# Kernel optimization log

Hardware: AMD Instinct MI355X
Metric: run time of the kernel (lower is better)

Reference implementation:

```python
import jax, jax.numpy as jnp
import numpy as np

N, H, T, HID = 2, 8, 1024, 64
EMBED_DIM = H * HID  # 512, out_proj dim
EPS = 1e-6


def setup_inputs() -> dict:
    key = jax.random.key(0)
    kq, kk, kv, kw, kb = jax.random.split(key, 5)
    q = jax.random.normal(kq, (N, H, T, HID), jnp.float32)
    k = jax.random.normal(kk, (N, H, T, HID), jnp.float32)
    v = jax.random.normal(kv, (N, H, T, HID), jnp.float32)
    W_out = jax.random.normal(kw, (EMBED_DIM, EMBED_DIM), jnp.float32) / np.float32(np.sqrt(EMBED_DIM))
    b_out = jax.random.normal(kb, (EMBED_DIM,), jnp.float32) * 0.02
    return {"q": q, "k": k, "v": v, "W_out": W_out, "b_out": b_out}


def reference(q, k, v, W_out, b_out):
    # cosFormer attention, causal=True, act_fun='relu', has_outproj=True
    n, h, t, hid = q.shape
    nh = n * h
    m = t  # max(src_len, tgt_len)

    # q/k: permute(2,0,1,3).view(T,N,H*HID) -> relu -> view(-1,N*H,HID).transpose(0,1)
    # is equivalent to a direct reshape (N,H,T,HID)->(N*H,T,HID) since relu is elementwise.
    qr = jax.nn.relu(q).reshape(nh, t, hid)
    kr = jax.nn.relu(k).reshape(nh, t, hid)
    # v: original does v.view(-1, N*H, HID).transpose(0,1) WITHOUT permuting first
    # (reinterprets the (N,H,T,HID) buffer as (T, N*H, HID)); reproduce faithfully.
    vr = jnp.swapaxes(v.reshape(t, nh, hid), 0, 1)  # (NH, T, HID)

    # cos/sin position reweighting: weight_index = pi/2 * arange(1..m), used as /m
    idx = (np.float32(np.pi / 2) * jnp.arange(1, t + 1, dtype=q.dtype)) / m  # (T,)
    s = jnp.sin(idx)[None, :, None]
    c = jnp.cos(idx)[None, :, None]
    q_ = jnp.concatenate([qr * s, qr * c], axis=-1)  # (NH, T, 2*HID)
    k_ = jnp.concatenate([kr * s, kr * c], axis=-1)  # (NH, T, 2*HID)

    # causal path: cumulative outer products k_ (x) v, then contract with q_
    kv = jnp.einsum('nld,nlm->nldm', k_, vr)          # (NH, T, 2*HID, HID)
    kv_cum = jnp.cumsum(kv, axis=1)
    qkv = jnp.einsum('nld,nldm->nlm', q_, kv_cum)     # (NH, T, HID)
    k_cum = jnp.cumsum(k_, axis=1)
    denom = jnp.maximum(jnp.einsum('nld,nld->nl', q_, k_cum), EPS)
    attn = qkv / denom[..., None]                     # (NH, T, HID)

    # (NH,T,HID) -> (T,N,H*HID), out_proj, back to (N,H,T,HID)
    attn = jnp.swapaxes(attn, 0, 1).reshape(t, n, h * hid)
    attn = attn @ W_out.T + b_out
    context = attn.reshape(t, n, h, hid).transpose(1, 2, 0, 3)  # (N,H,T,HID)
    probs = jnp.zeros((n, h, t, t), q.dtype)
    return context, probs
```

## Files before the change

kernel.cpp:

```cpp
#include <hip/hip_runtime.h>

#define TSEQ 1024
#define HIDV 64
#define NHEADS 16
#define LCH 64
#define NCH 16
#define EMBED 512
#define CTX_FLOATS (NHEADS * TSEQ * HIDV)
#define PROBS_F4 ((size_t)4194304)
#define EPSV 1e-6f
#define PIH 1.5707963267948966f

typedef short bf16x8 __attribute__((ext_vector_type(8)));
typedef float f32x4 __attribute__((ext_vector_type(4)));

__device__ __forceinline__ float relu_f(float x) { return fmaxf(x, 0.0f); }
__device__ __forceinline__ ushort f2bf(float f) {
    uint u = __float_as_uint(f);
    u += 0x7FFF + ((u >> 16) & 1);
    return (ushort)(u >> 16);
}
__device__ __forceinline__ float bf2f(ushort h) { return __uint_as_float(((uint)h) << 16); }
__device__ __forceinline__ uint pk2(float a, float b) {
    return (uint)f2bf(a) | ((uint)f2bf(b) << 16);
}

__global__ __launch_bounds__(512) void k_chunksum(
    const float* __restrict__ K, const float* __restrict__ V,
    float* __restrict__ Sws, float* __restrict__ ksumws,
    float4* __restrict__ probs4)
{
    __shared__ ushort kwT[128 * 72];
    __shared__ ushort vT[64 * 72];
    const int blk = blockIdx.x;
    const int b = blk >> 4, c = blk & 15;
    const int l0 = c * LCH;
    const int tid = threadIdx.x;

    {
        float4 z = make_float4(0.f, 0.f, 0.f, 0.f);
        size_t zb = (size_t)blk * 4096 + tid;
        #pragma unroll
        for (int s = 0; s < 8; ++s) probs4[zb + s * 512] = z;
    }

    #pragma unroll
    for (int s = 0; s < 2; ++s) {
        int e = tid + s * 512;
        int i = e >> 4, d = (e & 15) * 4;
        float4 k4 = *(const float4*)(K + (size_t)(b * TSEQ + l0 + i) * HIDV + d);
        float ang = PIH * (float)(l0 + i + 1) * (1.0f / 1024.0f);
        float si = sinf(ang), ci = cosf(ang);
        float kv[4] = {relu_f(k4.x), relu_f(k4.y), relu_f(k4.z), relu_f(k4.w)};
        #pragma unroll
        for (int j = 0; j < 4; ++j) {
            kwT[(d + j) * 72 + i] = f2bf(si * kv[j]);
            kwT[(d + 64 + j) * 72 + i] = f2bf(ci * kv[j]);
        }
        float4 v4 = *(const float4*)(V + ((size_t)(l0 + i) * NHEADS + b) * HIDV + d);
        float vv[4] = {v4.x, v4.y, v4.z, v4.w};
        #pragma unroll
        for (int j = 0; j < 4; ++j) vT[(d + j) * 72 + i] = f2bf(vv[j]);
    }
    __syncthreads();

    const int w = tid >> 6, lane = tid & 63;
    const int quad = lane >> 4, l15 = lane & 15;
    const int it = w;

    bf16x8 af[2];
    #pragma unroll
    for (int kk = 0; kk < 2; ++kk)
        af[kk] = *(const bf16x8*)(kwT + (it * 16 + l15) * 72 + kk * 32 + quad * 8);

    f32x4 acc[4];
    #pragma unroll
    for (int mt = 0; mt < 4; ++mt) {
        acc[mt] = (f32x4){0.f, 0.f, 0.f, 0.f};
        #pragma unroll
        for (int kk = 0; kk < 2; ++kk) {
            bf16x8 bf = *(const bf16x8*)(vT + (mt * 16 + l15) * 72 + kk * 32 + quad * 8);
            acc[mt] = __builtin_amdgcn_mfma_f32_16x16x32_bf16(af[kk], bf, acc[mt], 0, 0, 0);
        }
    }
    float* Sp = Sws + (size_t)blk * 8192;
    #pragma unroll
    for (int mt = 0; mt < 4; ++mt)
        #pragma unroll
        for (int r = 0; r < 4; ++r)
            Sp[(it * 16 + quad * 4 + r) * 64 + mt * 16 + l15] = acc[mt][r];

    if (tid < 128) {
        float s = 0.f;
        #pragma unroll
        for (int ss = 0; ss < 8; ++ss) {
            uint4 u = *(const uint4*)(kwT + tid * 72 + ss * 8);
            s += bf2f((ushort)(u.x & 0xffff)) + bf2f((ushort)(u.x >> 16));
            s += bf2f((ushort)(u.y & 0xffff)) + bf2f((ushort)(u.y >> 16));
            s += bf2f((ushort)(u.z & 0xffff)) + bf2f((ushort)(u.z >> 16));
            s += bf2f((ushort)(u.w & 0xffff)) + bf2f((ushort)(u.w >> 16));
        }
        ksumws[(size_t)blk * 128 + tid] = s;
    }
}

__global__ __launch_bounds__(256) void k_scan(
    float* __restrict__ Sws, float* __restrict__ ksumws,
    float4* __restrict__ probs4)
{
    {
        float4 z = make_float4(0.f, 0.f, 0.f, 0.f);
        size_t zb = 1048576 + (size_t)blockIdx.x * 2048 + threadIdx.x;
        #pragma unroll
        for (int s = 0; s < 8; ++s) probs4[zb + s * 256] = z;
    }
    int g = blockIdx.x * 256 + threadIdx.x;
    int b = g >> 13, idx = g & 8191;
    float acc = 0.0f;
    #pragma unroll
    for (int c = 0; c < NCH; ++c) {
        float* p = Sws + ((size_t)(b * NCH + c)) * 8192 + idx;
        float t = *p; *p = acc; acc += t;
    }
    if (g < NHEADS * 128) {
        int b2 = g >> 7, i2 = g & 127;
        float a2 = 0.0f;
        #pragma unroll
        for (int c = 0; c < NCH; ++c) {
            float* p = ksumws + (size_t)(b2 * NCH + c) * 128 + i2;
            float t = *p; *p = a2; a2 += t;
        }
    }
}

__global__ __launch_bounds__(512) void k_attn(
    const float* __restrict__ Q, const float* __restrict__ K,
    const float* __restrict__ V,
    const float* __restrict__ Sws, const float* __restrict__ ksumws,
    float* __restrict__ attn2, float4* __restrict__ probs4)
{
    __shared__ ushort qw[64 * 136];
    __shared__ ushort kw[64 * 136];
    __shared__ ushort Pt[64 * 136];
    __shared__ ushort vT[64 * 72];
    __shared__ ushort Am[64 * 72];
    __shared__ float psum[128], denA[64], denI[64];

    const int blk = blockIdx.x;
    const int b = blk >> 4, c = blk & 15;
    const int l0 = c * LCH;
    const int tid = threadIdx.x;

    {
        float4 z = make_float4(0.f, 0.f, 0.f, 0.f);
        size_t zb = 2097152 + (size_t)blk * 4096 + tid;
        #pragma unroll
        for (int s = 0; s < 8; ++s) probs4[zb + s * 512] = z;
    }
    if (tid < 64) denA[tid] = 0.f;

    #pragma unroll
    for (int s = 0; s < 2; ++s) {
        int e = tid + s * 512;
        int i = e >> 4, d = (e & 15) * 4;
        float ang = PIH * (float)(l0 + i + 1) * (1.0f / 1024.0f);
        float si = sinf(ang), ci = cosf(ang);
        float4 q4 = *(const float4*)(Q + (size_t)(b * TSEQ + l0 + i) * HIDV + d);
        float qv[4] = {relu_f(q4.x), relu_f(q4.y), relu_f(q4.z), relu_f(q4.w)};
        *(uint2*)(qw + i * 136 + d) = make_uint2(pk2(si * qv[0], si * qv[1]), pk2(si * qv[2], si * qv[3]));
        *(uint2*)(qw + i * 136 + 64 + d) = make_uint2(pk2(ci * qv[0], ci * qv[1]), pk2(ci * qv[2], ci * qv[3]));
        float4 k4 = *(const float4*)(K + (size_t)(b * TSEQ + l0 + i) * HIDV + d);
        float kv[4] = {relu_f(k4.x), relu_f(k4.y), relu_f(k4.z), relu_f(k4.w)};
        *(uint2*)(kw + i * 136 + d) = make_uint2(pk2(si * kv[0], si * kv[1]), pk2(si * kv[2], si * kv[3]));
        *(uint2*)(kw + i * 136 + 64 + d) = make_uint2(pk2(ci * kv[0], ci * kv[1]), pk2(ci * kv[2], ci * kv[3]));
        float4 v4 = *(const float4*)(V + ((size_t)(l0 + i) * NHEADS + b) * HIDV + d);
        float vv[4] = {v4.x, v4.y, v4.z, v4.w};
        #pragma unroll
        for (int j = 0; j < 4; ++j) vT[(d + j) * 72 + i] = f2bf(vv[j]);
    }
    {
        const float* Pg = Sws + (size_t)blk * 8192;
        #pragma unroll
        for (int s = 0; s < 4; ++s) {
            int e = tid + s * 512;
            int dd = e >> 4, m = (e & 15) * 4;
            float4 p4 = *(const float4*)(Pg + dd * 64 + m);
            float pv[4] = {p4.x, p4.y, p4.z, p4.w};
            #pragma unroll
            for (int j = 0; j < 4; ++j) Pt[(m + j) * 136 + dd] = f2bf(pv[j]);
        }
        if (tid < 128) psum[tid] = ksumws[(size_t)blk * 128 + tid];
    }
    __syncthreads();

    const int w = tid >> 6, lane = tid & 63;
    const int quad = lane >> 4, l15 = lane & 15;
    const int it = w >> 1;
    const int jb = (w & 1) * 2;

    bf16x8 af[4];
    #pragma unroll
    for (int kk = 0; kk < 4; ++kk)
        af[kk] = *(const bf16x8*)(qw + (it * 16 + l15) * 136 + kk * 32 + quad * 8);

    f32x4 accA[2];
    #pragma unroll
    for (int jj = 0; jj < 2; ++jj) {
        accA[jj] = (f32x4){0.f, 0.f, 0.f, 0.f};
        #pragma unroll
        for (int kk = 0; kk < 4; ++kk) {
            bf16x8 bf = *(const bf16x8*)(kw + ((jb + jj) * 16 + l15) * 136 + kk * 32 + quad * 8);
            accA[jj] = __builtin_amdgcn_mfma_f32_16x16x32_bf16(af[kk], bf, accA[jj], 0, 0, 0);
        }
    }
    {
        float rsum[4] = {0.f, 0.f, 0.f, 0.f};
        #pragma unroll
        for (int jj = 0; jj < 2; ++jj) {
            int j = (jb + jj) * 16 + l15;
            #pragma unroll
            for (int r = 0; r < 4; ++r) {
                int i = it * 16 + quad * 4 + r;
                float val = (j <= i) ? accA[jj][r] : 0.f;
                Am[i * 72 + j] = f2bf(val);
                rsum[r] += val;
            }
        }
        #pragma unroll
        for (int off = 1; off < 16; off <<= 1) {
            rsum[0] += __shfl_xor(rsum[0], off);
            rsum[1] += __shfl_xor(rsum[1], off);
            rsum[2] += __shfl_xor(rsum[2], off);
            rsum[3] += __shfl_xor(rsum[3], off);
        }
        if (l15 == 0) {
            #pragma unroll
            for (int r = 0; r < 4; ++r)
                atomicAdd(&denA[it * 16 + quad * 4 + r], rsum[r]);
        }
    }
    if (tid < 64) {
        float s = 0.f;
        #pragma unroll
        for (int ss = 0; ss < 16; ++ss) {
            uint4 u = *(const uint4*)(qw + tid * 136 + ss * 8);
            s += bf2f((ushort)(u.x & 0xffff)) * psum[ss * 8 + 0] + bf2f((ushort)(u.x >> 16)) * psum[ss * 8 + 1];
            s += bf2f((ushort)(u.y & 0xffff)) * psum[ss * 8 + 2] + bf2f((ushort)(u.y >> 16)) * psum[ss * 8 + 3];
            s += bf2f((ushort)(u.z & 0xffff)) * psum[ss * 8 + 4] + bf2f((ushort)(u.z >> 16)) * psum[ss * 8 + 5];
            s += bf2f((ushort)(u.w & 0xffff)) * psum[ss * 8 + 6] + bf2f((ushort)(u.w >> 16)) * psum[ss * 8 + 7];
        }
        denI[tid] = s;
    }
    __syncthreads();

    f32x4 accO[2];
    #pragma unroll
    for (int mm = 0; mm < 2; ++mm) {
        accO[mm] = (f32x4){0.f, 0.f, 0.f, 0.f};
        #pragma unroll
        for (int kk = 0; kk < 4; ++kk) {
            bf16x8 bp = *(const bf16x8*)(Pt + ((jb + mm) * 16 + l15) * 136 + kk * 32 + quad * 8);
            accO[mm] = __builtin_amdgcn_mfma_f32_16x16x32_bf16(af[kk], bp, accO[mm], 0, 0, 0);
        }
    }
    bf16x8 aA[2];
    #pragma unroll
    for (int kk = 0; kk < 2; ++kk)
        aA[kk] = *(const bf16x8*)(Am + (it * 16 + l15) * 72 + kk * 32 + quad * 8);
    #pragma unroll
    for (int mm = 0; mm < 2; ++mm)
        #pragma unroll
        for (int kk = 0; kk < 2; ++kk) {
            bf16x8 bv = *(const bf16x8*)(vT + ((jb + mm) * 16 + l15) * 72 + kk * 32 + quad * 8);
            accO[mm] = __builtin_amdgcn_mfma_f32_16x16x32_bf16(aA[kk], bv, accO[mm], 0, 0, 0);
        }

    const int nb = b >> 3, hh = b & 7;
    #pragma unroll
    for (int r = 0; r < 4; ++r) {
        int i = it * 16 + quad * 4 + r;
        float inv = 1.0f / fmaxf(denA[i] + denI[i], EPSV);
        #pragma unroll
        for (int mm = 0; mm < 2; ++mm) {
            int m = (jb + mm) * 16 + l15;
            size_t row = (size_t)((l0 + i) * 2 + nb);
            attn2[row * EMBED + hh * 64 + m] = accO[mm][r] * inv;
        }
    }
}

__global__ __launch_bounds__(256) void k_outproj(
    const float* __restrict__ A2, const float* __restrict__ W,
    const float* __restrict__ bias, float* __restrict__ ctx,
    float4* __restrict__ probs4)
{
    __shared__ ushort Ab[64 * 72];
    __shared__ ushort Bb[64 * 72];
    const int r0 = blockIdx.x * 64;
    const int e0 = blockIdx.y * 64;
    const int tid = threadIdx.x;
    const int blin = blockIdx.y * 32 + blockIdx.x;

    {
        float4 z = make_float4(0.f, 0.f, 0.f, 0.f);
        size_t zb = 3145728 + (size_t)blin * 4096 + tid;
        #pragma unroll
        for (int s = 0; s < 16; ++s) probs4[zb + s * 256] = z;
    }

    const int w = tid >> 6, lane = tid & 63;
    const int quad = lane >> 4, l15 = lane & 15;
    const int it = w;
    f32x4 acc[4];
    #pragma unroll
    for (int jt = 0; jt < 4; ++jt) acc[jt] = (f32x4){0.f, 0.f, 0.f, 0.f};

    for (int f0 = 0; f0 < EMBED; f0 += 64) {
        __syncthreads();
        #pragma unroll
        for (int s = 0; s < 4; ++s) {
            int e = tid + s * 256;
            int rr = e >> 4, ff = (e & 15) * 4;
            float4 a4 = *(const float4*)(A2 + (size_t)(r0 + rr) * EMBED + f0 + ff);
            *(uint2*)(Ab + rr * 72 + ff) = make_uint2(pk2(a4.x, a4.y), pk2(a4.z, a4.w));
            float4 w4 = *(const float4*)(W + (size_t)(e0 + rr) * EMBED + f0 + ff);
            *(uint2*)(Bb + rr * 72 + ff) = make_uint2(pk2(w4.x, w4.y), pk2(w4.z, w4.w));
        }
        __syncthreads();
        bf16x8 af[2];
        #pragma unroll
        for (int kk = 0; kk < 2; ++kk)
            af[kk] = *(const bf16x8*)(Ab + (it * 16 + l15) * 72 + kk * 32 + quad * 8);
        #pragma unroll
        for (int jt = 0; jt < 4; ++jt)
            #pragma unroll
            for (int kk = 0; kk < 2; ++kk) {
                bf16x8 bf = *(const bf16x8*)(Bb + (jt * 16 + l15) * 72 + kk * 32 + quad * 8);
                acc[jt] = __builtin_amdgcn_mfma_f32_16x16x32_bf16(af[kk], bf, acc[jt], 0, 0, 0);
            }
    }
    #pragma unroll
    for (int jt = 0; jt < 4; ++jt) {
        int e = e0 + jt * 16 + l15;
        float be = bias[e];
        int h = e >> 6, m = e & 63;
        #pragma unroll
        for (int r = 0; r < 4; ++r) {
            int rr = r0 + it * 16 + quad * 4 + r;
            int t = rr >> 1, n = rr & 1;
            ctx[((size_t)(n * 8 + h) * TSEQ + t) * HIDV + m] = acc[jt][r] + be;
        }
    }
}

extern "C" void kernel_launch(void* const* d_in, const int* in_sizes, int n_in,
                              void* d_out, int out_size, void* d_ws, size_t ws_size,
                              hipStream_t stream) {
    const float* q = (const float*)d_in[0];
    const float* k = (const float*)d_in[1];
    const float* v = (const float*)d_in[2];
    const float* W = (const float*)d_in[3];
    const float* bias = (const float*)d_in[4];
    float* out = (float*)d_out;
    float* ws = (float*)d_ws;

    float* S_ws = ws;
    float* ksum_ws = ws + 2097152;
    float* attn2 = ws + 2097152 + 32768;
    float4* probs4 = (float4*)(out + CTX_FLOATS);

    k_chunksum<<<dim3(256), dim3(512), 0, stream>>>(k, v, S_ws, ksum_ws, probs4);
    k_scan<<<dim3(512), dim3(256), 0, stream>>>(S_ws, ksum_ws, probs4);
    k_attn<<<dim3(256), dim3(512), 0, stream>>>(q, k, v, S_ws, ksum_ws, attn2, probs4);
    k_outproj<<<dim3(32, 8), dim3(256), 0, stream>>>(attn2, W, bias, out, probs4);
}
```

Before: 121.4 us.

## Fuse four attention stages into one cooperative persistent kernel with grid syncs

Replaces the four separate launches (chunk sums, scan, attention, out-projection) with one cooperative kernel of 512 blocks that uses grid.sync between phases. The chunk state is stored in bf16 and pre-transposed, so the attention phase loads it with vector copies. Work per block is re-split: attention now splits the output columns across two blocks, and the probs zero-fill is spread over idle blocks. This removes launch gaps and halves intermediate traffic, at the cost of grid-wide barriers, an occupancy requirement for co-residency, and lower precision in the scanned prefix sums.

```diff
diff --git a/kernel.cpp b/kernel.cpp
--- a/kernel.cpp
+++ b/kernel.cpp
@@ -1,4 +1,7 @@
 #include <hip/hip_runtime.h>
+#include <hip/hip_cooperative_groups.h>
+
+namespace cg = cooperative_groups;
 
 #define TSEQ 1024
 #define HIDV 64
@@ -7,7 +10,6 @@
 #define NCH 16
 #define EMBED 512
 #define CTX_FLOATS (NHEADS * TSEQ * HIDV)
-#define PROBS_F4 ((size_t)4194304)
 #define EPSV 1e-6f
 #define PIH 1.5707963267948966f
 
@@ -25,331 +27,339 @@
     return (uint)f2bf(a) | ((uint)f2bf(b) << 16);
 }
 
-__global__ __launch_bounds__(512) void k_chunksum(
-    const float* __restrict__ K, const float* __restrict__ V,
-    float* __restrict__ Sws, float* __restrict__ ksumws,
+#define SMEM_BYTES 58368
+#define OFF_QW 0
+#define OFF_KW 17408
+#define OFF_PT 34816
+#define OFF_VT 43520
+#define OFF_AM 48128
+#define OFF_PSUM 57344
+#define OFF_DENA 57856
+#define OFF_DENI 58112
+
+__global__ __launch_bounds__(256) void k_fused(
+    const float* __restrict__ Q, const float* __restrict__ K,
+    const float* __restrict__ V, const float* __restrict__ W,
+    const float* __restrict__ bias, float* __restrict__ out,
+    ushort* __restrict__ S16, float* __restrict__ ksumws,
+    ushort* __restrict__ Ptg, float* __restrict__ attn2,
     float4* __restrict__ probs4)
 {
-    __shared__ ushort kwT[128 * 72];
-    __shared__ ushort vT[64 * 72];
-    const int blk = blockIdx.x;
-    const int b = blk >> 4, c = blk & 15;
-    const int l0 = c * LCH;
+    __shared__ __align__(16) char smem[SMEM_BYTES];
+    cg::grid_group grid = cg::this_grid();
+
+    const int bid = blockIdx.x;
     const int tid = threadIdx.x;
+    const int w = tid >> 6, lane = tid & 63;
+    const int quad = lane >> 4, l15 = lane & 15;
+
+    if (bid < 256) {
+        ushort* kwT = (ushort*)smem;
+        ushort* vT1 = (ushort*)(smem + 22528);
+        const int pair = bid;
+        const int b = pair >> 4, c = pair & 15;
+        const int l0 = c * LCH;
+
+        #pragma unroll
+        for (int s = 0; s < 4; ++s) {
+            int e = tid + s * 256;
+            int i = e >> 4, d = (e & 15) * 4;
+            float4 k4 = *(const float4*)(K + (size_t)(b * TSEQ + l0 + i) * HIDV + d);
+            float si, ci;
+            __sincosf(PIH * (float)(l0 + i + 1) * (1.0f / 1024.0f), &si, &ci);
+            float kv[4] = {relu_f(k4.x), relu_f(k4.y), relu_f(k4.z), relu_f(k4.w)};
+            #pragma unroll
+            for (int j = 0; j < 4; ++j) {
+                kwT[(d + j) * 88 + i] = f2bf(si * kv[j]);
+                kwT[(d + 64 + j) * 88 + i] = f2bf(ci * kv[j]);
+            }
+            float4 v4 = *(const float4*)(V + ((size_t)(l0 + i) * NHEADS + b) * HIDV + d);
+            float vv[4] = {v4.x, v4.y, v4.z, v4.w};
+            #pragma unroll
+            for (int j = 0; j < 4; ++j) vT1[(d + j) * 88 + i] = f2bf(vv[j]);
+        }
+        __syncthreads();
+
+        f32x4 acc[2][4];
+        #pragma unroll
+        for (int ii = 0; ii < 2; ++ii)
+            #pragma unroll
+            for (int mt = 0; mt < 4; ++mt) acc[ii][mt] = (f32x4){0.f, 0.f, 0.f, 0.f};
+        #pragma unroll
+        for (int ii = 0; ii < 2; ++ii) {
+            int itv = w + ii * 4;
+            bf16x8 af[2];
+            #pragma unroll
+            for (int kk = 0; kk < 2; ++kk)
+                af[kk] = *(const bf16x8*)(kwT + (itv * 16 + l15) * 88 + kk * 32 + quad * 8);
+            #pragma unroll
+            for (int mt = 0; mt < 4; ++mt)
+                #pragma unroll
+                for (int kk = 0; kk < 2; ++kk) {
+                    bf16x8 bf = *(const bf16x8*)(vT1 + (mt * 16 + l15) * 88 + kk * 32 + quad * 8);
+                    acc[ii][mt] = __builtin_amdgcn_mfma_f32_16x16x32_bf16(af[kk], bf, acc[ii][mt], 0, 0, 0);
+                }
+        }
+        ushort* SpT = S16 + (size_t)pair * 8192;
+        #pragma unroll
+        for (int ii = 0; ii < 2; ++ii)
+            #pragma unroll
+            for (int mt = 0; mt < 4; ++mt) {
+                int m = mt * 16 + l15;
+                int ddb = (w + ii * 4) * 16 + quad * 4;
+                uint2 pk = make_uint2(pk2(acc[ii][mt][0], acc[ii][mt][1]),
+                                      pk2(acc[ii][mt][2], acc[ii][mt][3]));
+                *(uint2*)(SpT + m * 128 + ddb) = pk;
+            }
+        if (tid < 128) {
+            float ssum = 0.f;
+            #pragma unroll
+            for (int ss = 0; ss < 8; ++ss) {
+                uint4 u = *(const uint4*)(kwT + tid * 88 + ss * 8);
+                ssum += bf2f((ushort)(u.x & 0xffff)) + bf2f((ushort)(u.x >> 16));
+                ssum += bf2f((ushort)(u.y & 0xffff)) + bf2f((ushort)(u.y >> 16));
+                ssum += bf2f((ushort)(u.z & 0xffff)) + bf2f((ushort)(u.z >> 16));
+                ssum += bf2f((ushort)(u.w & 0xffff)) + bf2f((ushort)(u.w >> 16));
+            }
+            ksumws[(size_t)pair * 128 + tid] = ssum;
+        }
+    } else {
+        float4 z = make_float4(0.f, 0.f, 0.f, 0.f);
+        size_t base = (size_t)(bid - 256) * 8192 + tid;
+        #pragma unroll
+        for (int s = 0; s < 32; ++s) probs4[base + s * 256] = z;
+    }
+
+    grid.sync();
+
+    {
+        int g = bid * 256 + tid;
+        int bs = g >> 13, idx = g & 8191;
+        const ushort* Sp = S16 + (size_t)bs * 131072 + idx;
+        ushort* Pp = Ptg + (size_t)bs * 131072 + idx;
+        float acc = 0.f;
+        #pragma unroll
+        for (int c = 0; c < NCH; ++c) {
+            float t = bf2f(Sp[c * 8192]);
+            Pp[c * 8192] = f2bf(acc);
+            acc += t;
+        }
+        if (g < NHEADS * 128) {
+            int b2 = g >> 7, i2 = g & 127;
+            float a2 = 0.f;
+            #pragma unroll
+            for (int c = 0; c < NCH; ++c) {
+                float* p = ksumws + (size_t)(b2 * NCH + c) * 128 + i2;
+                float t = *p; *p = a2; a2 += t;
+            }
+        }
+    }
+
+    grid.sync();
+
+    {
+        ushort* qw = (ushort*)(smem + OFF_QW);
+        ushort* kw = (ushort*)(smem + OFF_KW);
+        ushort* Pt = (ushort*)(smem + OFF_PT);
+        ushort* vT = (ushort*)(smem + OFF_VT);
+        ushort* Am = (ushort*)(smem + OFF_AM);
+        float* psum = (float*)(smem + OFF_PSUM);
+        float* denA = (float*)(smem + OFF_DENA);
+        float* denI = (float*)(smem + OFF_DENI);
+
+        const int pair = bid >> 1, mh = bid & 1, m0b = mh * 32;
+        const int b = pair >> 4, c = pair & 15;
+        const int l0 = c * LCH;
+
+        #pragma unroll
+        for (int s = 0; s < 4; ++s) {
+            int e = tid + s * 256;
+            int i = e >> 4, d = (e & 15) * 4;
+            float si, ci;
+            __sincosf(PIH * (float)(l0 + i + 1) * (1.0f / 1024.0f), &si, &ci);
+            float4 q4 = *(const float4*)(Q + (size_t)(b * TSEQ + l0 + i) * HIDV + d);
+            float qv[4] = {relu_f(q4.x), relu_f(q4.y), relu_f(q4.z), relu_f(q4.w)};
+            *(uint2*)(qw + i * 136 + d) = make_uint2(pk2(si * qv[0], si * qv[1]), pk2(si * qv[2], si * qv[3]));
+            *(uint2*)(qw + i * 136 + 64 + d) = make_uint2(pk2(ci * qv[0], ci * qv[1]), pk2(ci * qv[2], ci * qv[3]));
+            float4 k4 = *(const float4*)(K + (size_t)(b * TSEQ + l0 + i) * HIDV + d);
+            float kv[4] = {relu_f(k4.x), relu_f(k4.y), relu_f(k4.z), relu_f(k4.w)};
+            *(uint2*)(kw + i * 136 + d) = make_uint2(pk2(si * kv[0], si * kv[1]), pk2(si * kv[2], si * kv[3]));
+            *(uint2*)(kw + i * 136 + 64 + d) = make_uint2(pk2(ci * kv[0], ci * kv[1]), pk2(ci * kv[2], ci * kv[3]));
+        }
+        {
+            const ushort* Pg = Ptg + (size_t)pair * 8192;
+            #pragma unroll
+            for (int s = 0; s < 2; ++s) {
+                int e = tid + s * 256;
+                int mrow = e >> 4, dd8 = (e & 15) * 8;
+                *(uint4*)(Pt + mrow * 136 + dd8) = *(const uint4*)(Pg + (m0b + mrow) * 128 + dd8);
+            }
+        }
+        #pragma unroll
+        for (int s = 0; s < 2; ++s) {
+            int e = tid + s * 256;
+            int j = e >> 3, mf = (e & 7) * 4;
+            float4 v4 = *(const float4*)(V + ((size_t)(l0 + j) * NHEADS + b) * HIDV + m0b + mf);
+            vT[(mf + 0) * 72 + j] = f2bf(v4.x);
+            vT[(mf + 1) * 72 + j] = f2bf(v4.y);
+            vT[(mf + 2) * 72 + j] = f2bf(v4.z);
+            vT[(mf + 3) * 72 + j] = f2bf(v4.w);
+        }
+        if (tid < 128) psum[tid] = ksumws[(size_t)pair * 128 + tid];
+        __syncthreads();
+
+        const int it = w;
+        bf16x8 af[4];
+        #pragma unroll
+        for (int kk = 0; kk < 4; ++kk)
+            af[kk] = *(const bf16x8*)(qw + (it * 16 + l15) * 136 + kk * 32 + quad * 8);
+
+        f32x4 accA[4];
+        #pragma unroll
+        for (int jt = 0; jt < 4; ++jt) {
+            accA[jt] = (f32x4){0.f, 0.f, 0.f, 0.f};
+            #pragma unroll
+            for (int kk = 0; kk < 4; ++kk) {
+                bf16x8 bf = *(const bf16x8*)(kw + (jt * 16 + l15) * 136 + kk * 32 + quad * 8);
+                accA[jt] = __builtin_amdgcn_mfma_f32_16x16x32_bf16(af[kk], bf, accA[jt], 0, 0, 0);
+            }
+        }
+        {
+            float rsum[4] = {0.f, 0.f, 0.f, 0.f};
+            #pragma unroll
+            for (int jt = 0; jt < 4; ++jt) {
+                int j = jt * 16 + l15;
+                #pragma unroll
+                for (int r = 0; r < 4; ++r) {
+                    int i = it * 16 + quad * 4 + r;
+                    float val = (j <= i) ? accA[jt][r] : 0.f;
+                    Am[i * 72 + j] = f2bf(val);
+                    rsum[r] += val;
+                }
+            }
+            #pragma unroll
+            for (int off = 1; off < 16; off <<= 1) {
+                rsum[0] += __shfl_xor(rsum[0], off);
+                rsum[1] += __shfl_xor(rsum[1], off);
+                rsum[2] += __shfl_xor(rsum[2], off);
+                rsum[3] += __shfl_xor(rsum[3], off);
+            }
+            if (l15 == 0) {
+                #pragma unroll
+                for (int r = 0; r < 4; ++r) denA[it * 16 + quad * 4 + r] = rsum[r];
+            }
+        }
+        if (tid < 64) {
+            float s = 0.f;
+            #pragma unroll
+            for (int ss = 0; ss < 16; ++ss) {
+                uint4 u = *(const uint4*)(qw + tid * 136 + ss * 8);
+                s += bf2f((ushort)(u.x & 0xffff)) * psum[ss * 8 + 0] + bf2f((ushort)(u.x >> 16)) * psum[ss * 8 + 1];
+                s += bf2f((ushort)(u.y & 0xffff)) * psum[ss * 8 + 2] + bf2f((ushort)(u.y >> 16)) * psum[ss * 8 + 3];
+                s += bf2f((ushort)(u.z & 0xffff)) * psum[ss * 8 + 4] + bf2f((ushort)(u.z >> 16)) * psum[ss * 8 + 5];
+                s += bf2f((ushort)(u.w & 0xffff)) * psum[ss * 8 + 6] + bf2f((ushort)(u.w >> 16)) * psum[ss * 8 + 7];
+            }
+            denI[tid] = s;
+        }
+        __syncthreads();
+
+        f32x4 accO[2];
+        #pragma unroll
+        for (int mm = 0; mm < 2; ++mm) {
+            accO[mm] = (f32x4){0.f, 0.f, 0.f, 0.f};
+            #pragma unroll
+            for (int kk = 0; kk < 4; ++kk) {
+                bf16x8 bp = *(const bf16x8*)(Pt + (mm * 16 + l15) * 136 + kk * 32 + quad * 8);
+                accO[mm] = __builtin_amdgcn_mfma_f32_16x16x32_bf16(af[kk], bp, accO[mm], 0, 0, 0);
+            }
+        }
+        bf16x8 aA[2];
+        #pragma unroll
+        for (int kk = 0; kk < 2; ++kk)
+            aA[kk] = *(const bf16x8*)(Am + (it * 16 + l15) * 72 + kk * 32 + quad * 8);
+        #pragma unroll
+        for (int mm = 0; mm < 2; ++mm)
+            #pragma unroll
+            for (int kk = 0; kk < 2; ++kk) {
+                bf16x8 bv = *(const bf16x8*)(vT + (mm * 16 + l15) * 72 + kk * 32 + quad * 8);
+                accO[mm] = __builtin_amdgcn_mfma_f32_16x16x32_bf16(aA[kk], bv, accO[mm], 0, 0, 0);
+            }
+
+        const int nb = b >> 3, hh = b & 7;
+        #pragma unroll
+        for (int r = 0; r < 4; ++r) {
+            int i = it * 16 + quad * 4 + r;
+            float inv = 1.0f / fmaxf(denA[i] + denI[i], EPSV);
+            #pragma unroll
+            for (int mm = 0; mm < 2; ++mm) {
+                int m = m0b + mm * 16 + l15;
+                attn2[(size_t)((l0 + i) * 2 + nb) * EMBED + hh * 64 + m] = accO[mm][r] * inv;
+            }
+        }
+    }
+
+    grid.sync();
+
+    {
+        ushort* Ab = (ushort*)smem;
+        ushort* Bb = (ushort*)(smem + 4608);
+        const int rt = bid >> 3, et = bid & 7;
+        const int r0 = rt * 32, e0 = et * 64;
+        const int it4 = w >> 1, jt0 = (w & 1) * 2;
+        f32x4 acc4[2];
+        acc4[0] = (f32x4){0.f, 0.f, 0.f, 0.f};
+        acc4[1] = (f32x4){0.f, 0.f, 0.f, 0.f};
+
+        for (int f0 = 0; f0 < EMBED; f0 += 64) {
+            __syncthreads();
+            #pragma unroll
+            for (int s = 0; s < 2; ++s) {
+                int e = tid + s * 256;
+                int rr = e >> 4, ff = (e & 15) * 4;
+                float4 a4 = *(const float4*)(attn2 + (size_t)(r0 + rr) * EMBED + f0 + ff);
+                *(uint2*)(Ab + rr * 72 + ff) = make_uint2(pk2(a4.x, a4.y), pk2(a4.z, a4.w));
+            }
+            #pragma unroll
+            for (int s = 0; s < 4; ++s) {
+                int e = tid + s * 256;
+                int rr = e >> 4, ff = (e & 15) * 4;
+                float4 w4 = *(const float4*)(W + (size_t)(e0 + rr) * EMBED + f0 + ff);
+                *(uint2*)(Bb + rr * 72 + ff) = make_uint2(pk2(w4.x, w4.y), pk2(w4.z, w4.w));
+            }
+            __syncthreads();
+            bf16x8 af2[2];
+            #pragma unroll
+            for (int kk = 0; kk < 2; ++kk)
+                af2[kk] = *(const bf16x8*)(Ab + (it4 * 16 + l15) * 72 + kk * 32 + quad * 8);
+            #pragma unroll
+            for (int jj = 0; jj < 2; ++jj) {
+                int jt = jt0 + jj;
+                #pragma unroll
+                for (int kk = 0; kk < 2; ++kk) {
+                    bf16x8 bf = *(const bf16x8*)(Bb + (jt * 16 + l15) * 72 + kk * 32 + quad * 8);
+                    acc4[jj] = __builtin_amdgcn_mfma_f32_16x16x32_bf16(af2[kk], bf, acc4[jj], 0, 0, 0);
+                }
+            }
+        }
+        #pragma unroll
+        for (int jj = 0; jj < 2; ++jj) {
+            int e = e0 + (jt0 + jj) * 16 + l15;
+            float be = bias[e];
+            int h = e >> 6, m = e & 63;
+            #pragma unroll
+            for (int r = 0; r < 4; ++r) {
+                int rr = r0 + it4 * 16 + quad * 4 + r;
+                int t = rr >> 1, n = rr & 1;
+                out[((size_t)(n * 8 + h) * TSEQ + t) * HIDV + m] = acc4[jj][r] + be;
+            }
+        }
+    }
 
     {
         float4 z = make_float4(0.f, 0.f, 0.f, 0.f);
-        size_t zb = (size_t)blk * 4096 + tid;
-        #pragma unroll
-        for (int s = 0; s < 8; ++s) probs4[zb + s * 512] = z;
-    }
-
-    #pragma unroll
-    for (int s = 0; s < 2; ++s) {
-        int e = tid + s * 512;
-        int i = e >> 4, d = (e & 15) * 4;
-        float4 k4 = *(const float4*)(K + (size_t)(b * TSEQ + l0 + i) * HIDV + d);
-        float ang = PIH * (float)(l0 + i + 1) * (1.0f / 1024.0f);
-        float si = sinf(ang), ci = cosf(ang);
-        float kv[4] = {relu_f(k4.x), relu_f(k4.y), relu_f(k4.z), relu_f(k4.w)};
-        #pragma unroll
-        for (int j = 0; j < 4; ++j) {
-            kwT[(d + j) * 72 + i] = f2bf(si * kv[j]);
-            kwT[(d + 64 + j) * 72 + i] = f2bf(ci * kv[j]);
-        }
-        float4 v4 = *(const float4*)(V + ((size_t)(l0 + i) * NHEADS + b) * HIDV + d);
-        float vv[4] = {v4.x, v4.y, v4.z, v4.w};
-        #pragma unroll
-        for (int j = 0; j < 4; ++j) vT[(d + j) * 72 + i] = f2bf(vv[j]);
-    }
-    __syncthreads();
-
-    const int w = tid >> 6, lane = tid & 63;
-    const int quad = lane >> 4, l15 = lane & 15;
-    const int it = w;
-
-    bf16x8 af[2];
-    #pragma unroll
-    for (int kk = 0; kk < 2; ++kk)
-        af[kk] = *(const bf16x8*)(kwT + (it * 16 + l15) * 72 + kk * 32 + quad * 8);
-
-    f32x4 acc[4];
-    #pragma unroll
-    for (int mt = 0; mt < 4; ++mt) {
-        acc[mt] = (f32x4){0.f, 0.f, 0.f, 0.f};
-        #pragma unroll
-        for (int kk = 0; kk < 2; ++kk) {
-            bf16x8 bf = *(const bf16x8*)(vT + (mt * 16 + l15) * 72 + kk * 32 + quad * 8);
-            acc[mt] = __builtin_amdgcn_mfma_f32_16x16x32_bf16(af[kk], bf, acc[mt], 0, 0, 0);
-        }
-    }
-    float* Sp = Sws + (size_t)blk * 8192;
-    #pragma unroll
-    for (int mt = 0; mt < 4; ++mt)
-        #pragma unroll
-        for (int r = 0; r < 4; ++r)
-            Sp[(it * 16 + quad * 4 + r) * 64 + mt * 16 + l15] = acc[mt][r];
-
-    if (tid < 128) {
-        float s = 0.f;
-        #pragma unroll
-        for (int ss = 0; ss < 8; ++ss) {
-            uint4 u = *(const uint4*)(kwT + tid * 72 + ss * 8);
-            s += bf2f((ushort)(u.x & 0xffff)) + bf2f((ushort)(u.x >> 16));
-            s += bf2f((ushort)(u.y & 0xffff)) + bf2f((ushort)(u.y >> 16));
-            s += bf2f((ushort)(u.z & 0xffff)) + bf2f((ushort)(u.z >> 16));
-            s += bf2f((ushort)(u.w & 0xffff)) + bf2f((ushort)(u.w >> 16));
-        }
-        ksumws[(size_t)blk * 128 + tid] = s;
-    }
-}
-
-__global__ __launch_bounds__(256) void k_scan(
-    float* __restrict__ Sws, float* __restrict__ ksumws,
-    float4* __restrict__ probs4)
-{
-    {
-        float4 z = make_float4(0.f, 0.f, 0.f, 0.f);
-        size_t zb = 1048576 + (size_t)blockIdx.x * 2048 + threadIdx.x;
-        #pragma unroll
-        for (int s = 0; s < 8; ++s) probs4[zb + s * 256] = z;
-    }
-    int g = blockIdx.x * 256 + threadIdx.x;
-    int b = g >> 13, idx = g & 8191;
-    float acc = 0.0f;
-    #pragma unroll
-    for (int c = 0; c < NCH; ++c) {
-        float* p = Sws + ((size_t)(b * NCH + c)) * 8192 + idx;
-        float t = *p; *p = acc; acc += t;
-    }
-    if (g < NHEADS * 128) {
-        int b2 = g >> 7, i2 = g & 127;
-        float a2 = 0.0f;
-        #pragma unroll
-        for (int c = 0; c < NCH; ++c) {
-            float* p = ksumws + (size_t)(b2 * NCH + c) * 128 + i2;
-            float t = *p; *p = a2; a2 += t;
-        }
-    }
-}
-
-__global__ __launch_bounds__(512) void k_attn(
-    const float* __restrict__ Q, const float* __restrict__ K,
-    const float* __restrict__ V,
-    const float* __restrict__ Sws, const float* __restrict__ ksumws,
-    float* __restrict__ attn2, float4* __restrict__ probs4)
-{
-    __shared__ ushort qw[64 * 136];
-    __shared__ ushort kw[64 * 136];
-    __shared__ ushort Pt[64 * 136];
-    __shared__ ushort vT[64 * 72];
-    __shared__ ushort Am[64 * 72];
-    __shared__ float psum[128], denA[64], denI[64];
-
-    const int blk = blockIdx.x;
-    const int b = blk >> 4, c = blk & 15;
-    const int l0 = c * LCH;
-    const int tid = threadIdx.x;
-
-    {
-        float4 z = make_float4(0.f, 0.f, 0.f, 0.f);
-        size_t zb = 2097152 + (size_t)blk * 4096 + tid;
-        #pragma unroll
-        for (int s = 0; s < 8; ++s) probs4[zb + s * 512] = z;
-    }
-    if (tid < 64) denA[tid] = 0.f;
-
-    #pragma unroll
-    for (int s = 0; s < 2; ++s) {
-        int e = tid + s * 512;
-        int i = e >> 4, d = (e & 15) * 4;
-        float ang = PIH * (float)(l0 + i + 1) * (1.0f / 1024.0f);
-        float si = sinf(ang), ci = cosf(ang);
-        float4 q4 = *(const float4*)(Q + (size_t)(b * TSEQ + l0 + i) * HIDV + d);
-        float qv[4] = {relu_f(q4.x), relu_f(q4.y), relu_f(q4.z), relu_f(q4.w)};
-        *(uint2*)(qw + i * 136 + d) = make_uint2(pk2(si * qv[0], si * qv[1]), pk2(si * qv[2], si * qv[3]));
-        *(uint2*)(qw + i * 136 + 64 + d) = make_uint2(pk2(ci * qv[0], ci * qv[1]), pk2(ci * qv[2], ci * qv[3]));
-        float4 k4 = *(const float4*)(K + (size_t)(b * TSEQ + l0 + i) * HIDV + d);
-        float kv[4] = {relu_f(k4.x), relu_f(k4.y), relu_f(k4.z), relu_f(k4.w)};
-        *(uint2*)(kw + i * 136 + d) = make_uint2(pk2(si * kv[0], si * kv[1]), pk2(si * kv[2], si * kv[3]));
-        *(uint2*)(kw + i * 136 + 64 + d) = make_uint2(pk2(ci * kv[0], ci * kv[1]), pk2(ci * kv[2], ci * kv[3]));
-        float4 v4 = *(const float4*)(V + ((size_t)(l0 + i) * NHEADS + b) * HIDV + d);
-        float vv[4] = {v4.x, v4.y, v4.z, v4.w};
-        #pragma unroll
-        for (int j = 0; j < 4; ++j) vT[(d + j) * 72 + i] = f2bf(vv[j]);
-    }
-    {
-        const float* Pg = Sws + (size_t)blk * 8192;
-        #pragma unroll
-        for (int s = 0; s < 4; ++s) {
-            int e = tid + s * 512;
-            int dd = e >> 4, m = (e & 15) * 4;
-            float4 p4 = *(const float4*)(Pg + dd * 64 + m);
-            float pv[4] = {p4.x, p4.y, p4.z, p4.w};
-            #pragma unroll
-            for (int j = 0; j < 4; ++j) Pt[(m + j) * 136 + dd] = f2bf(pv[j]);
-        }
-        if (tid < 128) psum[tid] = ksumws[(size_t)blk * 128 + tid];
-    }
-    __syncthreads();
-
-    const int w = tid >> 6, lane = tid & 63;
-    const int quad = lane >> 4, l15 = lane & 15;
-    const int it = w >> 1;
-    const int jb = (w & 1) * 2;
-
-    bf16x8 af[4];
-    #pragma unroll
-    for (int kk = 0; kk < 4; ++kk)
-        af[kk] = *(const bf16x8*)(qw + (it * 16 + l15) * 136 + kk * 32 + quad * 8);
-
-    f32x4 accA[2];
-    #pragma unroll
-    for (int jj = 0; jj < 2; ++jj) {
-        accA[jj] = (f32x4){0.f, 0.f, 0.f, 0.f};
-        #pragma unroll
-        for (int kk = 0; kk < 4; ++kk) {
-            bf16x8 bf = *(const bf16x8*)(kw + ((jb + jj) * 16 + l15) * 136 + kk * 32 + quad * 8);
-            accA[jj] = __builtin_amdgcn_mfma_f32_16x16x32_bf16(af[kk], bf, accA[jj], 0, 0, 0);
-        }
-    }
-    {
-        float rsum[4] = {0.f, 0.f, 0.f, 0.f};
-        #pragma unroll
-        for (int jj = 0; jj < 2; ++jj) {
-            int j = (jb + jj) * 16 + l15;
-            #pragma unroll
-            for (int r = 0; r < 4; ++r) {
-                int i = it * 16 + quad * 4 + r;
-                float val = (j <= i) ? accA[jj][r] : 0.f;
-                Am[i * 72 + j] = f2bf(val);
-                rsum[r] += val;
-            }
-        }
-        #pragma unroll
-        for (int off = 1; off < 16; off <<= 1) {
-            rsum[0] += __shfl_xor(rsum[0], off);
-            rsum[1] += __shfl_xor(rsum[1], off);
-            rsum[2] += __shfl_xor(rsum[2], off);
-            rsum[3] += __shfl_xor(rsum[3], off);
-        }
-        if (l15 == 0) {
-            #pragma unroll
-            for (int r = 0; r < 4; ++r)
-                atomicAdd(&denA[it * 16 + quad * 4 + r], rsum[r]);
-        }
-    }
-    if (tid < 64) {
-        float s = 0.f;
-        #pragma unroll
-        for (int ss = 0; ss < 16; ++ss) {
-            uint4 u = *(const uint4*)(qw + tid * 136 + ss * 8);
-            s += bf2f((ushort)(u.x & 0xffff)) * psum[ss * 8 + 0] + bf2f((ushort)(u.x >> 16)) * psum[ss * 8 + 1];
-            s += bf2f((ushort)(u.y & 0xffff)) * psum[ss * 8 + 2] + bf2f((ushort)(u.y >> 16)) * psum[ss * 8 + 3];
-            s += bf2f((ushort)(u.z & 0xffff)) * psum[ss * 8 + 4] + bf2f((ushort)(u.z >> 16)) * psum[ss * 8 + 5];
-            s += bf2f((ushort)(u.w & 0xffff)) * psum[ss * 8 + 6] + bf2f((ushort)(u.w >> 16)) * psum[ss * 8 + 7];
-        }
-        denI[tid] = s;
-    }
-    __syncthreads();
-
-    f32x4 accO[2];
-    #pragma unroll
-    for (int mm = 0; mm < 2; ++mm) {
-        accO[mm] = (f32x4){0.f, 0.f, 0.f, 0.f};
-        #pragma unroll
-        for (int kk = 0; kk < 4; ++kk) {
-            bf16x8 bp = *(const bf16x8*)(Pt + ((jb + mm) * 16 + l15) * 136 + kk * 32 + quad * 8);
-            accO[mm] = __builtin_amdgcn_mfma_f32_16x16x32_bf16(af[kk], bp, accO[mm], 0, 0, 0);
-        }
-    }
-    bf16x8 aA[2];
-    #pragma unroll
-    for (int kk = 0; kk < 2; ++kk)
-        aA[kk] = *(const bf16x8*)(Am + (it * 16 + l15) * 72 + kk * 32 + quad * 8);
-    #pragma unroll
-    for (int mm = 0; mm < 2; ++mm)
-        #pragma unroll
-        for (int kk = 0; kk < 2; ++kk) {
-            bf16x8 bv = *(const bf16x8*)(vT + ((jb + mm) * 16 + l15) * 72 + kk * 32 + quad * 8);
-            accO[mm] = __builtin_amdgcn_mfma_f32_16x16x32_bf16(aA[kk], bv, accO[mm], 0, 0, 0);
-        }
-
-    const int nb = b >> 3, hh = b & 7;
-    #pragma unroll
-    for (int r = 0; r < 4; ++r) {
-        int i = it * 16 + quad * 4 + r;
-        float inv = 1.0f / fmaxf(denA[i] + denI[i], EPSV);
-        #pragma unroll
-        for (int mm = 0; mm < 2; ++mm) {
-            int m = (jb + mm) * 16 + l15;
-            size_t row = (size_t)((l0 + i) * 2 + nb);
-            attn2[row * EMBED + hh * 64 + m] = accO[mm][r] * inv;
-        }
-    }
-}
-
-__global__ __launch_bounds__(256) void k_outproj(
-    const float* __restrict__ A2, const float* __restrict__ W,
-    const float* __restrict__ bias, float* __restrict__ ctx,
-    float4* __restrict__ probs4)
-{
-    __shared__ ushort Ab[64 * 72];
-    __shared__ ushort Bb[64 * 72];
-    const int r0 = blockIdx.x * 64;
-    const int e0 = blockIdx.y * 64;
-    const int tid = threadIdx.x;
-    const int blin = blockIdx.y * 32 + blockIdx.x;
-
-    {
-        float4 z = make_float4(0.f, 0.f, 0.f, 0.f);
-        size_t zb = 3145728 + (size_t)blin * 4096 + tid;
-        #pragma unroll
-        for (int s = 0; s < 16; ++s) probs4[zb + s * 256] = z;
-    }
-
-    const int w = tid >> 6, lane = tid & 63;
-    const int quad = lane >> 4, l15 = lane & 15;
-    const int it = w;
-    f32x4 acc[4];
-    #pragma unroll
-    for (int jt = 0; jt < 4; ++jt) acc[jt] = (f32x4){0.f, 0.f, 0.f, 0.f};
-
-    for (int f0 = 0; f0 < EMBED; f0 += 64) {
-        __syncthreads();
-        #pragma unroll
-        for (int s = 0; s < 4; ++s) {
-            int e = tid + s * 256;
-            int rr = e >> 4, ff = (e & 15) * 4;
-            float4 a4 = *(const float4*)(A2 + (size_t)(r0 + rr) * EMBED + f0 + ff);
-            *(uint2*)(Ab + rr * 72 + ff) = make_uint2(pk2(a4.x, a4.y), pk2(a4.z, a4.w));
-            float4 w4 = *(const float4*)(W + (size_t)(e0 + rr) * EMBED + f0 + ff);
-            *(uint2*)(Bb + rr * 72 + ff) = make_uint2(pk2(w4.x, w4.y), pk2(w4.z, w4.w));
-        }
-        __syncthreads();
-        bf16x8 af[2];
-        #pragma unroll
-        for (int kk = 0; kk < 2; ++kk)
-            af[kk] = *(const bf16x8*)(Ab + (it * 16 + l15) * 72 + kk * 32 + quad * 8);
-        #pragma unroll
-        for (int jt = 0; jt < 4; ++jt)
-            #pragma unroll
-            for (int kk = 0; kk < 2; ++kk) {
-                bf16x8 bf = *(const bf16x8*)(Bb + (jt * 16 + l15) * 72 + kk * 32 + quad * 8);
-                acc[jt] = __builtin_amdgcn_mfma_f32_16x16x32_bf16(af[kk], bf, acc[jt], 0, 0, 0);
-            }
-    }
-    #pragma unroll
-    for (int jt = 0; jt < 4; ++jt) {
-        int e = e0 + jt * 16 + l15;
-        float be = bias[e];
-        int h = e >> 6, m = e & 63;
-        #pragma unroll
-        for (int r = 0; r < 4; ++r) {
-            int rr = r0 + it * 16 + quad * 4 + r;
-            int t = rr >> 1, n = rr & 1;
-            ctx[((size_t)(n * 8 + h) * TSEQ + t) * HIDV + m] = acc[jt][r] + be;
-        }
+        size_t base = 2097152 + (size_t)bid * 4096 + tid;
+        #pragma unroll
+        for (int s = 0; s < 16; ++s) probs4[base + s * 256] = z;
     }
 }
 
@@ -364,13 +374,17 @@
     float* out = (float*)d_out;
     float* ws = (float*)d_ws;
 
-    float* S_ws = ws;
-    float* ksum_ws = ws + 2097152;
-    float* attn2 = ws + 2097152 + 32768;
+    ushort* S16 = (ushort*)ws;
+    float* ksum_ws = ws + 1048576;
+    ushort* Ptg = (ushort*)(ws + 1048576 + 32768);
+    float* attn2 = ws + 1048576 + 32768 + 1048576;
     float4* probs4 = (float4*)(out + CTX_FLOATS);
 
-    k_chunksum<<<dim3(256), dim3(512), 0, stream>>>(k, v, S_ws, ksum_ws, probs4);
-    k_scan<<<dim3(512), dim3(256), 0, stream>>>(S_ws, ksum_ws, probs4);
-    k_attn<<<dim3(256), dim3(512), 0, stream>>>(q, k, v, S_ws, ksum_ws, attn2, probs4);
-    k_outproj<<<dim3(32, 8), dim3(256), 0, stream>>>(attn2, W, bias, out, probs4);
+    void* args[] = {
+        (void*)&q, (void*)&k, (void*)&v, (void*)&W, (void*)&bias,
+        (void*)&out, (void*)&S16, (void*)&ksum_ws, (void*)&Ptg,
+        (void*)&attn2, (void*)&probs4
+    };
+    hipLaunchCooperativeKernel((const void*)k_fused, dim3(512), dim3(256),
+                               args, 0, stream);
 }
```

Result: slower. 309.5 us (+155.1%).
